# Performance work log

Hardware: AMD Instinct MI355X
Metric: run time of the kernel (lower is better)

The kernel has to match this reference:

```python
import jax, jax.numpy as jnp
import numpy as np

G1 = 8      # channel groups
G2 = 16     # spatial blocks per side
C1, C2 = 128, 64
H1 = W1 = 128
H2 = W2 = 256
BS1 = H1 // G2   # 8  -> 64 elems per x1 block
BS2 = H2 // G2   # 16 -> 256 elems per x2 block
BN_EPS = 1e-5


def setup_inputs() -> dict:
    key = jax.random.key(0)
    ks = jax.random.split(key, 16)
    B = 4
    c1g, c2g = C1 // G1, C2 // G1          # 16, 8
    inp = {
        "x1": jax.random.normal(ks[0], (B, C1, H1, W1), jnp.float32),
        "x2": jax.random.normal(ks[1], (B, C2, H2, W2), jnp.float32),
        # Conv1: conv1d k=1, C1//G1 -> C1//2//G1  (16 -> 8)
        "w_c1": jax.random.normal(ks[2], (c1g // 2, c1g), jnp.float32) * 0.1,
        "b_c1": jnp.zeros((c1g // 2,), jnp.float32),
        # Conv2: conv1d k=1, C2//G1 -> C2//G1  (8 -> 8)
        "w_c2": jax.random.normal(ks[3], (c2g, c2g), jnp.float32) * 0.1,
        "b_c2": jnp.zeros((c2g,), jnp.float32),
        # conv1 / conv2: 1x1 conv2d to 1 channel
        "w_p1": jax.random.normal(ks[4], (C1,), jnp.float32) * 0.1,
        "b_p1": jnp.zeros((), jnp.float32),
        "w_p2": jax.random.normal(ks[5], (C2,), jnp.float32) * 0.1,
        "b_p2": jnp.zeros((), jnp.float32),
        # SpatialAttention linear: 64 -> 256 (torch weight layout [out, in])
        "w_lin": jax.random.normal(ks[6], (BS2 * BS2, BS1 * BS1), jnp.float32) * 0.1,
        "b_lin": jnp.zeros((BS2 * BS2,), jnp.float32),
        # convbnrelu: 1x1 conv C2->C2 + BN (eval mode, running stats mean=0 var=1)
        "w_f": jax.random.normal(ks[7], (C2, C2), jnp.float32) * 0.05,
        "b_f": jnp.zeros((C2,), jnp.float32),
        "bn_gamma": jnp.ones((C2,), jnp.float32),
        "bn_beta": jnp.zeros((C2,), jnp.float32),
    }
    return inp


def reference(x1, x2, w_c1, b_c1, w_c2, b_c2, w_p1, b_p1, w_p2, b_p2,
              w_lin, b_lin, w_f, b_f, bn_gamma, bn_beta):
    B = x1.shape[0]
    c1g, c2g = C1 // G1, C2 // G1

    # ---- grouped channel attention (vectorized over the 8 groups) ----
    gap1 = x1.reshape(B, G1, c1g, H1 * W1).mean(-1)           # [B,g,16]
    gap2 = x2.reshape(B, G1, c2g, H2 * W2).mean(-1)           # [B,g,8]
    mlp1 = jax.nn.relu(jnp.einsum('oc,bgc->bgo', w_c1, gap1) + b_c1)  # [B,g,8]
    mlp2 = jax.nn.relu(jnp.einsum('oc,bgc->bgo', w_c2, gap2) + b_c2)  # [B,g,8]
    sem = jnp.einsum('bgo,bgp->bgop', mlp1, mlp2)             # [B,g,8,8]
    cw_logits = jnp.einsum('bgop,bgp->bgo', sem, mlp2)        # [B,g,8]
    cw = jax.nn.softmax(cw_logits, axis=-1)                   # softmax over channel dim
    sem_x2 = (x2.reshape(B, G1, c2g, H2, W2) * cw[..., None, None]
              ).reshape(B, C2, H2, W2)

    # ---- block-wise spatial attention (vectorized over 16x16 blocks) ----
    nb = G2 * G2
    x1b = x1.reshape(B, C1, G2, BS1, G2, BS1).transpose(0, 2, 4, 1, 3, 5)
    x1b = x1b.reshape(B, nb, C1, BS1, BS1)
    x2b = x2.reshape(B, C2, G2, BS2, G2, BS2).transpose(0, 2, 4, 1, 3, 5)
    x2b = x2b.reshape(B, nb, C2, BS2, BS2)

    pos1 = (jnp.einsum('c,bncij->bnij', w_p1, x1b) + b_p1).reshape(B, nb, BS1 * BS1)
    pos2 = (jnp.einsum('c,bncij->bnij', w_p2, x2b) + b_p2).reshape(B, nb, BS2 * BS2)

    x1t = jnp.einsum('oc,bnc->bno', w_lin, pos1) + b_lin      # [B,nb,256]
    # bmm(x2^T, x1t) is an outer product since both are rank-1 per block
    scores = pos2[..., :, None] * x1t[..., None, :]           # [B,nb,256,256]
    aw = jax.nn.softmax(scores, axis=-1)
    weighted = jnp.einsum('bnq,bnqk->bnk', pos2, aw)          # [B,nb,256]
    # torch.cat(dim=2).view(B,1,H2,W2): raw row-major flatten of block outputs
    spa = weighted.reshape(B, 1, H2, W2)

    # ---- fuse: 1x1 conv + BN(eval) + ReLU ----
    pre = sem_x2 + spa
    conv = jnp.einsum('oc,bchw->bohw', w_f, pre) + b_f[:, None, None]
    bn = conv / jnp.sqrt(jnp.float32(1.0 + BN_EPS)) * bn_gamma[:, None, None] \
         + bn_beta[:, None, None]
    return jax.nn.relu(bn)
```

## Files before the change

kernel.cpp:

```cpp
#include <hip/hip_runtime.h>


#define GAP_OFF  0
#define POS1_OFF 768
#define POS2_OFF 66304

typedef __attribute__((ext_vector_type(8))) short short8;
typedef __attribute__((ext_vector_type(4))) float f32x4;
union U8 { short8 s; unsigned int u[4]; };

__global__ __launch_bounds__(256) void k_fuse(const float* __restrict__ x1,
                                              const float* __restrict__ x2,
                                              const float* __restrict__ w_p1,
                                              const float* __restrict__ b_p1,
                                              const float* __restrict__ w_p2,
                                              const float* __restrict__ b_p2,
                                              float* __restrict__ ws) {
  __shared__ float gbuf[64 * 65];
  __shared__ float pbuf[1024];
  int blk = blockIdx.x, t = threadIdx.x;
  int wv = t >> 6, ln = t & 63;
  if (blk < 256) {
    int b = blk >> 6;
    int px0 = (blk & 63) << 8;
    const float* xb = x1 + ((size_t)b << 21) + px0 + (ln << 2);
    float4 pacc; pacc.x = pacc.y = pacc.z = pacc.w = 0.f;
    float gs[32];
#pragma unroll
    for (int i = 0; i < 32; ++i) {
      int c = (i << 2) + wv;
      float4 v = *(const float4*)(xb + ((size_t)c << 14));
      float wc = w_p1[c];
      pacc.x = fmaf(wc, v.x, pacc.x); pacc.y = fmaf(wc, v.y, pacc.y);
      pacc.z = fmaf(wc, v.z, pacc.z); pacc.w = fmaf(wc, v.w, pacc.w);
      gs[i] = (v.x + v.y) + (v.z + v.w);
    }
#pragma unroll
    for (int i = 0; i < 16; ++i) gbuf[((wv << 4) + i) * 65 + ln] = gs[i];
    *(float4*)&pbuf[(wv << 8) + (ln << 2)] = pacc;
    __syncthreads();
    if (t < 64) {
      const float* gp = &gbuf[t * 65];
      float s0 = 0.f, s1 = 0.f, s2 = 0.f, s3 = 0.f;
#pragma unroll
      for (int k = 0; k < 64; k += 4) { s0 += gp[k]; s1 += gp[k+1]; s2 += gp[k+2]; s3 += gp[k+3]; }
      atomicAdd(&ws[GAP_OFF + b * 128 + ((t & 15) << 2) + (t >> 4)], (s0 + s1) + (s2 + s3));
    }
    float s = (pbuf[t] + pbuf[256 + t]) + (pbuf[512 + t] + pbuf[768 + t]) + b_p1[0];
    int p = px0 + t, h = p >> 7, w0 = p & 127;
    int n = ((h >> 3) << 4) + (w0 >> 3);
    ws[POS1_OFF + ((b * 256 + n) << 6) + ((h & 7) << 3) + (w0 & 7)] = s;
    __syncthreads();
#pragma unroll
    for (int i = 16; i < 32; ++i) gbuf[((wv << 4) + (i - 16)) * 65 + ln] = gs[i];
    __syncthreads();
    if (t < 64) {
      const float* gp = &gbuf[t * 65];
      float s0 = 0.f, s1 = 0.f, s2 = 0.f, s3 = 0.f;
#pragma unroll
      for (int k = 0; k < 64; k += 4) { s0 += gp[k]; s1 += gp[k+1]; s2 += gp[k+2]; s3 += gp[k+3]; }
      atomicAdd(&ws[GAP_OFF + b * 128 + 64 + ((t & 15) << 2) + (t >> 4)], (s0 + s1) + (s2 + s3));
    }
  } else {
    int j = blk - 256;
    int b = j >> 8;
    int row = j & 255;
    const float* xb = x2 + ((size_t)b << 22) + (row << 8) + (ln << 2);
    float4 pacc; pacc.x = pacc.y = pacc.z = pacc.w = 0.f;
    float gs[16];
#pragma unroll
    for (int i = 0; i < 16; ++i) {
      int c = (i << 2) + wv;
      float4 v = *(const float4*)(xb + ((size_t)c << 16));
      float wc = w_p2[c];
      pacc.x = fmaf(wc, v.x, pacc.x); pacc.y = fmaf(wc, v.y, pacc.y);
      pacc.z = fmaf(wc, v.z, pacc.z); pacc.w = fmaf(wc, v.w, pacc.w);
      gs[i] = (v.x + v.y) + (v.z + v.w);
    }
#pragma unroll
    for (int i = 0; i < 16; ++i) gbuf[((wv << 4) + i) * 65 + ln] = gs[i];
    *(float4*)&pbuf[(wv << 8) + (ln << 2)] = pacc;
    __syncthreads();
    if (t < 64) {
      int w2 = t >> 4, i2 = t & 15;
      int c = (i2 << 2) + w2;
      const float* gp = &gbuf[t * 65];
      float s0 = 0.f, s1 = 0.f, s2 = 0.f, s3 = 0.f;
#pragma unroll
      for (int k = 0; k < 64; k += 4) { s0 += gp[k]; s1 += gp[k+1]; s2 += gp[k+2]; s3 += gp[k+3]; }
      atomicAdd(&ws[GAP_OFF + 512 + b * 64 + c], (s0 + s1) + (s2 + s3));
    }
    float s = (pbuf[t] + pbuf[256 + t]) + (pbuf[512 + t] + pbuf[768 + t]) + b_p2[0];
    int n = ((row >> 4) << 4) + (t >> 4);
    ws[POS2_OFF + ((b * 256 + n) << 8) + ((row & 15) << 4) + (t & 15)] = s;
  }
}

__global__ __launch_bounds__(256) void k_mrg(const float* __restrict__ x2,
                                             const float* __restrict__ w_lin,
                                             const float* __restrict__ b_lin,
                                             const float* __restrict__ w_c1,
                                             const float* __restrict__ b_c1,
                                             const float* __restrict__ w_c2,
                                             const float* __restrict__ b_c2,
                                             const float* __restrict__ w_f,
                                             const float* __restrict__ b_f,
                                             const float* __restrict__ gm,
                                             const float* __restrict__ bt,
                                             const float* __restrict__ ws,
                                             float* __restrict__ out) {
  __shared__ unsigned short aHi[4096];
  __shared__ float P1[64], V[256], A2[256], T[256], spa_s[256];
  __shared__ float g1s[128], g2s[64], cw_l[64], p2s[64], p3s[64];
  const float L2E = 1.44269504088896f;
  const float kbn = 0.99999500003749969f;
  int t = threadIdx.x;
  int blk = blockIdx.x;
  int b = blk >> 8, n = blk & 255;

  if (t < 128) g1s[t] = ws[GAP_OFF + b * 128 + t] * (1.f / 16384.f);
  if (t < 64)  g2s[t] = ws[GAP_OFF + 512 + b * 64 + t] * (1.f / 65536.f);
  if (t < 64)  P1[t] = ws[POS1_OFF + blk * 64 + t];
  float a = ws[POS2_OFF + blk * 256 + t];
  float a2 = a * L2E;
  A2[t] = a2;
  if (t < 64) {
    const float4* wrow = (const float4*)(w_f + t * 64);
    float s0 = 0.f, s1 = 0.f, s2 = 0.f, s3 = 0.f;
#pragma unroll
    for (int k = 0; k < 16; ++k) {
      float4 wv = wrow[k];
      s0 += wv.x; s1 += wv.y; s2 += wv.z; s3 += wv.w;
    }
    float A = kbn * gm[t];
    p2s[t] = ((s0 + s1) + (s2 + s3)) * A;
    p3s[t] = fmaf(b_f[t], A, bt[t]);
  }
  __syncthreads();

  int l = t & 63;
  int wq = t >> 6;
  int pcol = l & 15;
  int krow = l >> 4;
  const float* xbase = x2 + ((size_t)b << 22) + (n << 8) + (wq << 6) + pcol
                       + ((size_t)(krow << 3) << 16);
  float xv[4][2][8];
#pragma unroll
  for (int jt = 0; jt < 4; ++jt)
#pragma unroll
    for (int ks = 0; ks < 2; ++ks)
#pragma unroll
      for (int j = 0; j < 8; ++j)
        xv[jt][ks][j] = xbase[(jt << 4) + ((size_t)((ks << 5) + j) << 16)];

  float v = b_lin[t];
  const float* wr = w_lin + t * 64;
#pragma unroll 16
  for (int c = 0; c < 64; ++c) v = fmaf(wr[c], P1[c], v);
  V[t] = v;
  if (t < 8) {
    int g = t;
    const float* g1 = g1s + g * 16;
    const float* g2 = g2s + g * 8;
    float m1[8];
    for (int o = 0; o < 8; ++o) {
      float s = b_c1[o];
      for (int c = 0; c < 16; ++c) s = fmaf(w_c1[o * 16 + c], g1[c], s);
      m1[o] = fmaxf(s, 0.f);
    }
    float ss = 0.f;
    for (int p = 0; p < 8; ++p) {
      float s = b_c2[p];
      for (int c = 0; c < 8; ++c) s = fmaf(w_c2[p * 8 + c], g2[c], s);
      float r = fmaxf(s, 0.f);
      ss = fmaf(r, r, ss);
    }
    float lg[8], mx = -1e30f;
    for (int o = 0; o < 8; ++o) { lg[o] = m1[o] * ss; mx = fmaxf(mx, lg[o]); }
    float se = 0.f;
    for (int o = 0; o < 8; ++o) {
      lg[o] = __builtin_amdgcn_exp2f((lg[o] - mx) * L2E);
      se += lg[o];
    }
    float inv = 1.f / se;
    for (int o = 0; o < 8; ++o) cw_l[g * 8 + o] = lg[o] * inv;
  }
  U8 bh[4][2], bl[4][2];
#pragma unroll
  for (int jt = 0; jt < 4; ++jt)
#pragma unroll
    for (int ks = 0; ks < 2; ++ks)
#pragma unroll
      for (int q = 0; q < 4; ++q) {
        float f0 = xv[jt][ks][2 * q], f1 = xv[jt][ks][2 * q + 1];
        unsigned int u0 = __float_as_uint(f0), u1 = __float_as_uint(f1);
        unsigned int h0 = u0 & 0xFFFF0000u, h1 = u1 & 0xFFFF0000u;
        bh[jt][ks].u[q] = (u0 >> 16) | h1;
        float e0 = f0 - __uint_as_float(h0);
        float e1 = f1 - __uint_as_float(h1);
        bl[jt][ks].u[q] = (__float_as_uint(e0) >> 16) | (__float_as_uint(e1) & 0xFFFF0000u);
      }
  __syncthreads();

  {
    unsigned int* aU = (unsigned int*)aHi;
#pragma unroll
    for (int gi = 0; gi < 4; ++gi) {
      int o = (gi << 4) + ((t >> 2) & 15);
      float ga = kbn * gm[o];
#pragma unroll
      for (int gk = 0; gk < 2; ++gk) {
        int c = (gk << 5) + ((t >> 6) << 3) + ((t & 3) << 1);
        float2 wf2 = *(const float2*)(w_f + (o << 6) + c);
        float v0 = wf2.x * cw_l[c] * ga;
        float v1 = wf2.y * cw_l[c + 1] * ga;
        unsigned int u0 = __float_as_uint(v0), u1 = __float_as_uint(v1);
        unsigned int r0 = (u0 + 0x7FFFu + ((u0 >> 16) & 1u)) >> 16;
        unsigned int r1 = (u1 + 0x7FFFu + ((u1 >> 16) & 1u)) & 0xFFFF0000u;
        aU[(((gi << 1) + gk) << 8) + t] = r0 | r1;
      }
    }
  }
  float d0 = 0.f, d1 = 0.f, d2 = 0.f, d3 = 0.f;
#pragma unroll 4
  for (int k = 0; k < 256; k += 4) {
    float4 vv = *(float4*)&V[k];
    d0 += __builtin_amdgcn_exp2f(a2 * vv.x);
    d1 += __builtin_amdgcn_exp2f(a2 * vv.y);
    d2 += __builtin_amdgcn_exp2f(a2 * vv.z);
    d3 += __builtin_amdgcn_exp2f(a2 * vv.w);
  }
  float den = (d0 + d1) + (d2 + d3);
  T[t] = a / den;
  __syncthreads();

  short8 afr[4][2];
#pragma unroll
  for (int i = 0; i < 4; ++i)
#pragma unroll
    for (int ks = 0; ks < 2; ++ks)
      afr[i][ks] = *(const short8*)&aHi[(((i << 1) + ks) << 9) + (l << 3)];
  float c0 = 0.f, c1 = 0.f, c2 = 0.f, c3 = 0.f;
#pragma unroll 4
  for (int q = 0; q < 256; q += 4) {
    float4 aq = *(float4*)&A2[q];
    float4 tq = *(float4*)&T[q];
    c0 = fmaf(tq.x, __builtin_amdgcn_exp2f(aq.x * v), c0);
    c1 = fmaf(tq.y, __builtin_amdgcn_exp2f(aq.y * v), c1);
    c2 = fmaf(tq.z, __builtin_amdgcn_exp2f(aq.z * v), c2);
    c3 = fmaf(tq.w, __builtin_amdgcn_exp2f(aq.w * v), c3);
  }
  spa_s[t] = (c0 + c1) + (c2 + c3);
  __syncthreads();

  float* obase = out + ((size_t)b << 22) + (n << 8) + (wq << 6) + pcol;
#pragma unroll
  for (int jt = 0; jt < 4; ++jt) {
    float spa_p = spa_s[(wq << 6) + (jt << 4) + pcol];
#pragma unroll
    for (int i = 0; i < 4; ++i) {
      f32x4 acc = {};
#pragma unroll
      for (int ks = 0; ks < 2; ++ks) {
        acc = __builtin_amdgcn_mfma_f32_16x16x32_bf16(afr[i][ks], bh[jt][ks].s, acc, 0, 0, 0);
        acc = __builtin_amdgcn_mfma_f32_16x16x32_bf16(afr[i][ks], bl[jt][ks].s, acc, 0, 0, 0);
      }
#pragma unroll
      for (int r = 0; r < 4; ++r) {
        int o = (i << 4) + (krow << 2) + r;
        float val = fmaf(spa_p, p2s[o], acc[r] + p3s[o]);
        obase[(jt << 4) + ((size_t)o << 16)] = fmaxf(val, 0.f);
      }
    }
  }
}

extern "C" void kernel_launch(void* const* d_in, const int* in_sizes, int n_in,
                              void* d_out, int out_size, void* d_ws, size_t ws_size,
                              hipStream_t stream) {
  const float* x1   = (const float*)d_in[0];
  const float* x2   = (const float*)d_in[1];
  const float* w_c1 = (const float*)d_in[2];
  const float* b_c1 = (const float*)d_in[3];
  const float* w_c2 = (const float*)d_in[4];
  const float* b_c2 = (const float*)d_in[5];
  const float* w_p1 = (const float*)d_in[6];
  const float* b_p1 = (const float*)d_in[7];
  const float* w_p2 = (const float*)d_in[8];
  const float* b_p2 = (const float*)d_in[9];
  const float* w_lin= (const float*)d_in[10];
  const float* b_lin= (const float*)d_in[11];
  const float* w_f  = (const float*)d_in[12];
  const float* b_f  = (const float*)d_in[13];
  const float* gmm  = (const float*)d_in[14];
  const float* btt  = (const float*)d_in[15];
  float* ws  = (float*)d_ws;
  float* out = (float*)d_out;

  hipMemsetAsync(ws, 0, 768 * sizeof(float), stream);
  hipLaunchKernelGGL(k_fuse, dim3(1280), dim3(256), 0, stream, x1, x2, w_p1, b_p1, w_p2, b_p2, ws);
  hipLaunchKernelGGL(k_mrg,  dim3(1024), dim3(256), 0, stream, x2, w_lin, b_lin,
                     w_c1, b_c1, w_c2, b_c2, w_f, b_f, gmm, btt, ws, out);
}
```

Measured before the change: 210.7 us.

## Process two spatial blocks per k_mrg workgroup and simplify x1 GAP reduction

k_mrg now handles two blocks per workgroup on half the grid. Each workgroup shares the w_lin row loads, the channel-attention MLP, the w_f A-fragment setup and the p2/p3 precompute across both blocks, and interleaves the two softmax pipelines to give more independent exp2 work. The x2 loads for the MFMA stage move from an early prefetch into a per-tile loop after the softmax, which lowers register pressure (launch bounds now ask for 2 blocks per SIMD) but no longer hides those load latencies behind the exp work. In k_fuse, the x1 GAP reduction uses a larger LDS buffer so a single pass with 128 threads replaces two passes with extra barriers.

```diff
diff --git a/kernel.cpp b/kernel.cpp
--- a/kernel.cpp
+++ b/kernel.cpp
@@ -16,7 +16,7 @@
                                               const float* __restrict__ w_p2,
                                               const float* __restrict__ b_p2,
                                               float* __restrict__ ws) {
-  __shared__ float gbuf[64 * 65];
+  __shared__ float gbuf[128 * 65];
   __shared__ float pbuf[1024];
   int blk = blockIdx.x, t = threadIdx.x;
   int wv = t >> 6, ln = t & 63;
@@ -36,31 +36,22 @@
       gs[i] = (v.x + v.y) + (v.z + v.w);
     }
 #pragma unroll
-    for (int i = 0; i < 16; ++i) gbuf[((wv << 4) + i) * 65 + ln] = gs[i];
+    for (int i = 0; i < 32; ++i) gbuf[((wv << 5) + i) * 65 + ln] = gs[i];
     *(float4*)&pbuf[(wv << 8) + (ln << 2)] = pacc;
     __syncthreads();
-    if (t < 64) {
+    if (t < 128) {
+      int w2 = t >> 5, i2 = t & 31;
+      int c = (i2 << 2) + w2;
       const float* gp = &gbuf[t * 65];
       float s0 = 0.f, s1 = 0.f, s2 = 0.f, s3 = 0.f;
 #pragma unroll
       for (int k = 0; k < 64; k += 4) { s0 += gp[k]; s1 += gp[k+1]; s2 += gp[k+2]; s3 += gp[k+3]; }
-      atomicAdd(&ws[GAP_OFF + b * 128 + ((t & 15) << 2) + (t >> 4)], (s0 + s1) + (s2 + s3));
+      atomicAdd(&ws[GAP_OFF + b * 128 + c], (s0 + s1) + (s2 + s3));
     }
     float s = (pbuf[t] + pbuf[256 + t]) + (pbuf[512 + t] + pbuf[768 + t]) + b_p1[0];
     int p = px0 + t, h = p >> 7, w0 = p & 127;
     int n = ((h >> 3) << 4) + (w0 >> 3);
     ws[POS1_OFF + ((b * 256 + n) << 6) + ((h & 7) << 3) + (w0 & 7)] = s;
-    __syncthreads();
-#pragma unroll
-    for (int i = 16; i < 32; ++i) gbuf[((wv << 4) + (i - 16)) * 65 + ln] = gs[i];
-    __syncthreads();
-    if (t < 64) {
-      const float* gp = &gbuf[t * 65];
-      float s0 = 0.f, s1 = 0.f, s2 = 0.f, s3 = 0.f;
-#pragma unroll
-      for (int k = 0; k < 64; k += 4) { s0 += gp[k]; s1 += gp[k+1]; s2 += gp[k+2]; s3 += gp[k+3]; }
-      atomicAdd(&ws[GAP_OFF + b * 128 + 64 + ((t & 15) << 2) + (t >> 4)], (s0 + s1) + (s2 + s3));
-    }
   } else {
     int j = blk - 256;
     int b = j >> 8;
@@ -96,34 +87,42 @@
   }
 }
 
-__global__ __launch_bounds__(256) void k_mrg(const float* __restrict__ x2,
-                                             const float* __restrict__ w_lin,
-                                             const float* __restrict__ b_lin,
-                                             const float* __restrict__ w_c1,
-                                             const float* __restrict__ b_c1,
-                                             const float* __restrict__ w_c2,
-                                             const float* __restrict__ b_c2,
-                                             const float* __restrict__ w_f,
-                                             const float* __restrict__ b_f,
-                                             const float* __restrict__ gm,
-                                             const float* __restrict__ bt,
-                                             const float* __restrict__ ws,
-                                             float* __restrict__ out) {
+__global__ __launch_bounds__(256, 2) void k_mrg(const float* __restrict__ x2,
+                                                const float* __restrict__ w_lin,
+                                                const float* __restrict__ b_lin,
+                                                const float* __restrict__ w_c1,
+                                                const float* __restrict__ b_c1,
+                                                const float* __restrict__ w_c2,
+                                                const float* __restrict__ b_c2,
+                                                const float* __restrict__ w_f,
+                                                const float* __restrict__ b_f,
+                                                const float* __restrict__ gm,
+                                                const float* __restrict__ bt,
+                                                const float* __restrict__ ws,
+                                                float* __restrict__ out) {
   __shared__ unsigned short aHi[4096];
-  __shared__ float P1[64], V[256], A2[256], T[256], spa_s[256];
+  __shared__ float P1a[64], P1b[64];
+  __shared__ float V0[256], V1[256], A20[256], A21[256], T0[256], T1[256];
+  __shared__ float sp0[256], sp1[256];
   __shared__ float g1s[128], g2s[64], cw_l[64], p2s[64], p3s[64];
   const float L2E = 1.44269504088896f;
   const float kbn = 0.99999500003749969f;
   int t = threadIdx.x;
   int blk = blockIdx.x;
-  int b = blk >> 8, n = blk & 255;
+  int b = blk >> 7;
+  int np = (blk & 127) << 1;
+  int rowg = (b << 8) + np;
 
   if (t < 128) g1s[t] = ws[GAP_OFF + b * 128 + t] * (1.f / 16384.f);
   if (t < 64)  g2s[t] = ws[GAP_OFF + 512 + b * 64 + t] * (1.f / 65536.f);
-  if (t < 64)  P1[t] = ws[POS1_OFF + blk * 64 + t];
-  float a = ws[POS2_OFF + blk * 256 + t];
-  float a2 = a * L2E;
-  A2[t] = a2;
+  if (t < 128) {
+    int r = t >> 6, c = t & 63;
+    (r ? P1b : P1a)[c] = ws[POS1_OFF + ((rowg + r) << 6) + c];
+  }
+  float a0 = ws[POS2_OFF + (rowg << 8) + t];
+  float a1 = ws[POS2_OFF + ((rowg + 1) << 8) + t];
+  float a20 = a0 * L2E, a21 = a1 * L2E;
+  A20[t] = a20; A21[t] = a21;
   if (t < 64) {
     const float4* wrow = (const float4*)(w_f + t * 64);
     float s0 = 0.f, s1 = 0.f, s2 = 0.f, s3 = 0.f;
@@ -138,26 +137,19 @@
   }
   __syncthreads();
 
-  int l = t & 63;
-  int wq = t >> 6;
-  int pcol = l & 15;
-  int krow = l >> 4;
-  const float* xbase = x2 + ((size_t)b << 22) + (n << 8) + (wq << 6) + pcol
-                       + ((size_t)(krow << 3) << 16);
-  float xv[4][2][8];
-#pragma unroll
-  for (int jt = 0; jt < 4; ++jt)
-#pragma unroll
-    for (int ks = 0; ks < 2; ++ks)
-#pragma unroll
-      for (int j = 0; j < 8; ++j)
-        xv[jt][ks][j] = xbase[(jt << 4) + ((size_t)((ks << 5) + j) << 16)];
-
-  float v = b_lin[t];
-  const float* wr = w_lin + t * 64;
-#pragma unroll 16
-  for (int c = 0; c < 64; ++c) v = fmaf(wr[c], P1[c], v);
-  V[t] = v;
+  float v0 = b_lin[t], v1 = v0;
+  const float4* wr4 = (const float4*)(w_lin + t * 64);
+#pragma unroll
+  for (int k = 0; k < 16; ++k) {
+    float4 wv = wr4[k];
+    float4 pa = *(float4*)&P1a[k << 2];
+    float4 pb = *(float4*)&P1b[k << 2];
+    v0 = fmaf(wv.x, pa.x, v0); v0 = fmaf(wv.y, pa.y, v0);
+    v0 = fmaf(wv.z, pa.z, v0); v0 = fmaf(wv.w, pa.w, v0);
+    v1 = fmaf(wv.x, pb.x, v1); v1 = fmaf(wv.y, pb.y, v1);
+    v1 = fmaf(wv.z, pb.z, v1); v1 = fmaf(wv.w, pb.w, v1);
+  }
+  V0[t] = v0; V1[t] = v1;
   if (t < 8) {
     int g = t;
     const float* g1 = g1s + g * 16;
@@ -185,21 +177,6 @@
     float inv = 1.f / se;
     for (int o = 0; o < 8; ++o) cw_l[g * 8 + o] = lg[o] * inv;
   }
-  U8 bh[4][2], bl[4][2];
-#pragma unroll
-  for (int jt = 0; jt < 4; ++jt)
-#pragma unroll
-    for (int ks = 0; ks < 2; ++ks)
-#pragma unroll
-      for (int q = 0; q < 4; ++q) {
-        float f0 = xv[jt][ks][2 * q], f1 = xv[jt][ks][2 * q + 1];
-        unsigned int u0 = __float_as_uint(f0), u1 = __float_as_uint(f1);
-        unsigned int h0 = u0 & 0xFFFF0000u, h1 = u1 & 0xFFFF0000u;
-        bh[jt][ks].u[q] = (u0 >> 16) | h1;
-        float e0 = f0 - __uint_as_float(h0);
-        float e1 = f1 - __uint_as_float(h1);
-        bl[jt][ks].u[q] = (__float_as_uint(e0) >> 16) | (__float_as_uint(e1) & 0xFFFF0000u);
-      }
   __syncthreads();
 
   {
@@ -212,64 +189,107 @@
       for (int gk = 0; gk < 2; ++gk) {
         int c = (gk << 5) + ((t >> 6) << 3) + ((t & 3) << 1);
         float2 wf2 = *(const float2*)(w_f + (o << 6) + c);
-        float v0 = wf2.x * cw_l[c] * ga;
-        float v1 = wf2.y * cw_l[c + 1] * ga;
-        unsigned int u0 = __float_as_uint(v0), u1 = __float_as_uint(v1);
+        float q0 = wf2.x * cw_l[c] * ga;
+        float q1 = wf2.y * cw_l[c + 1] * ga;
+        unsigned int u0 = __float_as_uint(q0), u1 = __float_as_uint(q1);
         unsigned int r0 = (u0 + 0x7FFFu + ((u0 >> 16) & 1u)) >> 16;
         unsigned int r1 = (u1 + 0x7FFFu + ((u1 >> 16) & 1u)) & 0xFFFF0000u;
         aU[(((gi << 1) + gk) << 8) + t] = r0 | r1;
       }
     }
   }
-  float d0 = 0.f, d1 = 0.f, d2 = 0.f, d3 = 0.f;
+  float d00 = 0.f, d01 = 0.f, d02 = 0.f, d03 = 0.f;
+  float d10 = 0.f, d11 = 0.f, d12 = 0.f, d13 = 0.f;
 #pragma unroll 4
   for (int k = 0; k < 256; k += 4) {
-    float4 vv = *(float4*)&V[k];
-    d0 += __builtin_amdgcn_exp2f(a2 * vv.x);
-    d1 += __builtin_amdgcn_exp2f(a2 * vv.y);
-    d2 += __builtin_amdgcn_exp2f(a2 * vv.z);
-    d3 += __builtin_amdgcn_exp2f(a2 * vv.w);
-  }
-  float den = (d0 + d1) + (d2 + d3);
-  T[t] = a / den;
+    float4 u = *(float4*)&V0[k];
+    d00 += __builtin_amdgcn_exp2f(a20 * u.x);
+    d01 += __builtin_amdgcn_exp2f(a20 * u.y);
+    d02 += __builtin_amdgcn_exp2f(a20 * u.z);
+    d03 += __builtin_amdgcn_exp2f(a20 * u.w);
+    float4 w = *(float4*)&V1[k];
+    d10 += __builtin_amdgcn_exp2f(a21 * w.x);
+    d11 += __builtin_amdgcn_exp2f(a21 * w.y);
+    d12 += __builtin_amdgcn_exp2f(a21 * w.z);
+    d13 += __builtin_amdgcn_exp2f(a21 * w.w);
+  }
+  T0[t] = a0 / ((d00 + d01) + (d02 + d03));
+  T1[t] = a1 / ((d10 + d11) + (d12 + d13));
   __syncthreads();
 
+  int l = t & 63;
+  int wq = t >> 6;
+  int pcol = l & 15;
+  int krow = l >> 4;
   short8 afr[4][2];
 #pragma unroll
   for (int i = 0; i < 4; ++i)
 #pragma unroll
     for (int ks = 0; ks < 2; ++ks)
       afr[i][ks] = *(const short8*)&aHi[(((i << 1) + ks) << 9) + (l << 3)];
-  float c0 = 0.f, c1 = 0.f, c2 = 0.f, c3 = 0.f;
+  float c00 = 0.f, c01 = 0.f, c02 = 0.f, c03 = 0.f;
+  float c10 = 0.f, c11 = 0.f, c12 = 0.f, c13 = 0.f;
 #pragma unroll 4
   for (int q = 0; q < 256; q += 4) {
-    float4 aq = *(float4*)&A2[q];
-    float4 tq = *(float4*)&T[q];
-    c0 = fmaf(tq.x, __builtin_amdgcn_exp2f(aq.x * v), c0);
-    c1 = fmaf(tq.y, __builtin_amdgcn_exp2f(aq.y * v), c1);
-    c2 = fmaf(tq.z, __builtin_amdgcn_exp2f(aq.z * v), c2);
-    c3 = fmaf(tq.w, __builtin_amdgcn_exp2f(aq.w * v), c3);
-  }
-  spa_s[t] = (c0 + c1) + (c2 + c3);
+    float4 aq = *(float4*)&A20[q];
+    float4 tq = *(float4*)&T0[q];
+    c00 = fmaf(tq.x, __builtin_amdgcn_exp2f(aq.x * v0), c00);
+    c01 = fmaf(tq.y, __builtin_amdgcn_exp2f(aq.y * v0), c01);
+    c02 = fmaf(tq.z, __builtin_amdgcn_exp2f(aq.z * v0), c02);
+    c03 = fmaf(tq.w, __builtin_amdgcn_exp2f(aq.w * v0), c03);
+    float4 ar = *(float4*)&A21[q];
+    float4 tr = *(float4*)&T1[q];
+    c10 = fmaf(tr.x, __builtin_amdgcn_exp2f(ar.x * v1), c10);
+    c11 = fmaf(tr.y, __builtin_amdgcn_exp2f(ar.y * v1), c11);
+    c12 = fmaf(tr.z, __builtin_amdgcn_exp2f(ar.z * v1), c12);
+    c13 = fmaf(tr.w, __builtin_amdgcn_exp2f(ar.w * v1), c13);
+  }
+  sp0[t] = (c00 + c01) + (c02 + c03);
+  sp1[t] = (c10 + c11) + (c12 + c13);
   __syncthreads();
 
-  float* obase = out + ((size_t)b << 22) + (n << 8) + (wq << 6) + pcol;
-#pragma unroll
-  for (int jt = 0; jt < 4; ++jt) {
-    float spa_p = spa_s[(wq << 6) + (jt << 4) + pcol];
-#pragma unroll
-    for (int i = 0; i < 4; ++i) {
-      f32x4 acc = {};
-#pragma unroll
-      for (int ks = 0; ks < 2; ++ks) {
-        acc = __builtin_amdgcn_mfma_f32_16x16x32_bf16(afr[i][ks], bh[jt][ks].s, acc, 0, 0, 0);
-        acc = __builtin_amdgcn_mfma_f32_16x16x32_bf16(afr[i][ks], bl[jt][ks].s, acc, 0, 0, 0);
-      }
-#pragma unroll
-      for (int r = 0; r < 4; ++r) {
-        int o = (i << 4) + (krow << 2) + r;
-        float val = fmaf(spa_p, p2s[o], acc[r] + p3s[o]);
-        obase[(jt << 4) + ((size_t)o << 16)] = fmaxf(val, 0.f);
+  for (int r = 0; r < 2; ++r) {
+    const float* xg = x2 + ((size_t)b << 22) + ((np + r) << 8) + (wq << 6) + pcol
+                      + ((size_t)(krow << 3) << 16);
+    const float* sps = r ? sp1 : sp0;
+    float* ob = out + ((size_t)b << 22) + ((np + r) << 8) + (wq << 6) + pcol;
+#pragma unroll
+    for (int jt = 0; jt < 4; ++jt) {
+      const float* xp = xg + (jt << 4);
+      float xv[2][8];
+#pragma unroll
+      for (int ks = 0; ks < 2; ++ks)
+#pragma unroll
+        for (int j = 0; j < 8; ++j)
+          xv[ks][j] = xp[(size_t)((ks << 5) + j) << 16];
+      U8 bh[2], bl[2];
+#pragma unroll
+      for (int ks = 0; ks < 2; ++ks)
+#pragma unroll
+        for (int q = 0; q < 4; ++q) {
+          float f0 = xv[ks][2 * q], f1 = xv[ks][2 * q + 1];
+          unsigned int u0 = __float_as_uint(f0), u1 = __float_as_uint(f1);
+          unsigned int h0 = u0 & 0xFFFF0000u, h1 = u1 & 0xFFFF0000u;
+          bh[ks].u[q] = (u0 >> 16) | h1;
+          float e0 = f0 - __uint_as_float(h0);
+          float e1 = f1 - __uint_as_float(h1);
+          bl[ks].u[q] = (__float_as_uint(e0) >> 16) | (__float_as_uint(e1) & 0xFFFF0000u);
+        }
+      float spa_p = sps[(wq << 6) + (jt << 4) + pcol];
+#pragma unroll
+      for (int i = 0; i < 4; ++i) {
+        f32x4 acc = {};
+#pragma unroll
+        for (int ks = 0; ks < 2; ++ks) {
+          acc = __builtin_amdgcn_mfma_f32_16x16x32_bf16(afr[i][ks], bh[ks].s, acc, 0, 0, 0);
+          acc = __builtin_amdgcn_mfma_f32_16x16x32_bf16(afr[i][ks], bl[ks].s, acc, 0, 0, 0);
+        }
+#pragma unroll
+        for (int rr = 0; rr < 4; ++rr) {
+          int o = (i << 4) + (krow << 2) + rr;
+          float val = fmaf(spa_p, p2s[o], acc[rr] + p3s[o]);
+          ob[(jt << 4) + ((size_t)o << 16)] = fmaxf(val, 0.f);
+        }
       }
     }
   }
@@ -299,6 +319,6 @@
 
   hipMemsetAsync(ws, 0, 768 * sizeof(float), stream);
   hipLaunchKernelGGL(k_fuse, dim3(1280), dim3(256), 0, stream, x1, x2, w_p1, b_p1, w_p2, b_p2, ws);
-  hipLaunchKernelGGL(k_mrg,  dim3(1024), dim3(256), 0, stream, x2, w_lin, b_lin,
+  hipLaunchKernelGGL(k_mrg,  dim3(512),  dim3(256), 0, stream, x2, w_lin, b_lin,
                      w_c1, b_c1, w_c2, b_c2, w_f, b_f, gmm, btt, ws, out);
 }
```

Measured after the change: 213.5 us. About the same (+1.3%).
